# Kernel tuning notes

Measured on AMD Instinct MI355X. Metric: run time of the kernel, lower is better.

The kernel has to match this reference:

```python
import jax, jax.numpy as jnp
import numpy as np

N_NODES = 21
LN_EPS = 1e-5


def setup_inputs() -> dict:
    key = jax.random.key(0)
    ks = jax.random.split(key, 10)
    B, d, gh, E = 8192, 256, 512, 40
    h = jax.random.normal(ks[0], (B, N_NODES, d), dtype=jnp.float32)
    src_index = jax.random.randint(ks[1], (E,), 0, N_NODES)
    dst_index = jax.random.randint(ks[2], (E,), 0, N_NODES)
    # LayerNorm params
    ln_w = jnp.ones((d,), jnp.float32)
    ln_b = jnp.zeros((d,), jnp.float32)
    # value_proj: Linear(d, d), stored as (in, out)
    Wv = jax.random.normal(ks[3], (d, d), dtype=jnp.float32) / np.sqrt(d)
    bv = jax.random.normal(ks[4], (d,), dtype=jnp.float32) * 0.01
    # gate_mlp: Linear(2d, gh) -> GELU -> Linear(gh, 1)
    W1 = jax.random.normal(ks[5], (2 * d, gh), dtype=jnp.float32) / np.sqrt(2 * d)
    b1 = jax.random.normal(ks[6], (gh,), dtype=jnp.float32) * 0.01
    W2 = jax.random.normal(ks[7], (gh, 1), dtype=jnp.float32) / np.sqrt(gh)
    b2 = jax.random.normal(ks[8], (1,), dtype=jnp.float32) * 0.01
    return {"h": h, "src_index": src_index, "dst_index": dst_index,
            "ln_w": ln_w, "ln_b": ln_b, "Wv": Wv, "bv": bv,
            "W1": W1, "b1": b1, "W2": W2, "b2": b2}


def _layernorm(x, w, b):
    mu = jnp.mean(x, axis=-1, keepdims=True)
    var = jnp.mean(jnp.square(x - mu), axis=-1, keepdims=True)
    return (x - mu) * jax.lax.rsqrt(var + LN_EPS) * w + b


def reference(h, src_index, dst_index, ln_w, ln_b, Wv, bv, W1, b1, W2, b2):
    residual = h
    x = _layernorm(h, ln_w, ln_b)                      # (B, 21, d)
    src_feat = x[:, src_index, :]                      # (B, E, d) gather
    dst_feat = x[:, dst_index, :]                      # (B, E, d) gather
    values = jnp.einsum('bed,df->bef', src_feat, Wv) + bv  # (B, E, d)
    g = jnp.concatenate([src_feat, dst_feat], axis=-1) # (B, E, 2d)
    g = jax.nn.gelu(jnp.einsum('bec,ch->beh', g, W1) + b1, approximate=False)
    gates = jax.nn.sigmoid(jnp.einsum('beh,ho->beo', g, W2) + b2)  # (B, E, 1)
    messages = gates * values                          # (B, E, d)
    aggregated = jnp.zeros_like(x).at[:, dst_index, :].add(messages)  # scatter-add over nodes
    return residual + aggregated
```

## Files before the change

### kernel.cpp

```cpp
#include <hip/hip_runtime.h>
#include <hip/hip_bf16.h>
#include <math.h>

typedef __attribute__((ext_vector_type(8))) short short8;
typedef __attribute__((ext_vector_type(4))) float f32x4;

#define NN    21
#define DD    256
#define GH    512
#define NE    40
#define BT    3
#define MROWS (BT * NN)
#define MPAD  64
#define NTHR  256
#define UVSTR 36

__device__ __forceinline__ f32x4 mfma16(short8 a, short8 b, f32x4 c) {
    return __builtin_amdgcn_mfma_f32_16x16x32_bf16(a, b, c, 0, 0, 0);
}

__global__ void prep_weights(const float* __restrict__ Wv, const float* __restrict__ W1,
                             __hip_bfloat16* __restrict__ WvT,
                             __hip_bfloat16* __restrict__ WtT,
                             __hip_bfloat16* __restrict__ WbT) {
    __shared__ float tile[64][65];
    int bi = blockIdx.x;
    const float* src;
    int ld, tc, th;
    bool isW1 = bi < 64;
    if (isW1) { src = W1; ld = 512; tc = (bi & 7) * 64; th = (bi >> 3) * 64; }
    else      { int b = bi - 64; src = Wv; ld = 256; tc = (b & 3) * 64; th = (b >> 2) * 64; }
    for (int i = 0; i < 16; ++i) {
        int e = threadIdx.x + 256 * i;
        int r = e >> 6, cc = e & 63;
        tile[r][cc] = src[(size_t)(tc + r) * ld + th + cc];
    }
    __syncthreads();
    for (int i = 0; i < 16; ++i) {
        int e  = threadIdx.x + 256 * i;
        int r2 = e >> 6, cc2 = e & 63;
        float v = tile[cc2][r2];
        int hh = th + r2, c = tc + cc2;
        if (isW1) {
            if (c < 256) WtT[hh * 256 + c]         = __float2bfloat16(v);
            else         WbT[hh * 256 + (c - 256)] = __float2bfloat16(v);
        } else {
            WvT[hh * 256 + c] = __float2bfloat16(v);
        }
    }
}

__launch_bounds__(NTHR, 3)
__global__ void fused_kernel(const float* __restrict__ hin,
                             const int* __restrict__ srci, const int* __restrict__ dsti,
                             const float* __restrict__ lnw, const float* __restrict__ lnb,
                             const float* __restrict__ bv,  const float* __restrict__ b1,
                             const float* __restrict__ W2,  const float* __restrict__ b2,
                             const __hip_bfloat16* __restrict__ WvT,
                             const __hip_bfloat16* __restrict__ WtT,
                             const __hip_bfloat16* __restrict__ WbT,
                             float* __restrict__ out, int Btotal) {
    __shared__ __align__(16) char smem[32768];
    __shared__ float b1s[GH], w2s[GH], bvs[DD];
    __shared__ float gates[BT * NE];
    __shared__ int   srcs[NE], dsts[NE];
    __shared__ int   csr_off[NN + 1], csr_cur[NN], csr_eid[NE];

    const int tid  = threadIdx.x;
    const int lane = tid & 63;
    const int w    = tid >> 6;
    const int b0   = blockIdx.x * BT;

    if (tid < NE) { srcs[tid] = srci[tid]; dsts[tid] = dsti[tid]; }
    b1s[tid] = b1[tid];  b1s[tid + 256] = b1[tid + 256];
    w2s[tid] = W2[tid];  w2s[tid + 256] = W2[tid + 256];
    bvs[tid] = bv[tid];
    if (tid <= NN) csr_off[tid] = 0;
    int myd = (tid < NE) ? dsti[tid] : 0;
    __syncthreads();
    if (tid < NE) atomicAdd(&csr_off[myd + 1], 1);

    {
        float4 wgt = ((const float4*)lnw)[lane];
        float4 bta = ((const float4*)lnb)[lane];
        for (int r = w; r < MPAD; r += 4) {
            int b_loc = r / NN;
            int node  = r - b_loc * NN;
            bool valid = (r < MROWS) && (b0 + b_loc < Btotal);
            float4 h4 = {0.f, 0.f, 0.f, 0.f};
            if (valid)
                h4 = *(const float4*)(hin + ((size_t)(b0 + b_loc) * NN + node) * DD + lane * 4);
            float s  = h4.x + h4.y + h4.z + h4.w;
            float ss = h4.x*h4.x + h4.y*h4.y + h4.z*h4.z + h4.w*h4.w;
            for (int off = 32; off; off >>= 1) {
                s  += __shfl_xor(s,  off);
                ss += __shfl_xor(ss, off);
            }
            float mu   = s * (1.0f / 256.0f);
            float rstd = rsqrtf(ss * (1.0f / 256.0f) - mu * mu + 1e-5f);
            __align__(8) __hip_bfloat16 t[4];
            if (valid) {
                t[0] = __float2bfloat16((h4.x - mu) * rstd * wgt.x + bta.x);
                t[1] = __float2bfloat16((h4.y - mu) * rstd * wgt.y + bta.y);
                t[2] = __float2bfloat16((h4.z - mu) * rstd * wgt.z + bta.z);
                t[3] = __float2bfloat16((h4.w - mu) * rstd * wgt.w + bta.w);
            } else {
                __hip_bfloat16 z = __float2bfloat16(0.0f);
                t[0] = z; t[1] = z; t[2] = z; t[3] = z;
            }
            char* dst = smem + r * 512 + ((((lane >> 1) ^ (r & 7)) << 4) | ((lane & 1) << 3));
            *(ushort4*)dst = *(ushort4*)&t[0];
        }
    }
    __syncthreads();

    if (tid == 0) {
        for (int n = 0; n < NN; ++n) csr_off[n + 1] += csr_off[n];
        for (int n = 0; n < NN; ++n) csr_cur[n] = csr_off[n];
        for (int e = 0; e < NE; ++e) { int d = dsts[e]; csr_eid[csr_cur[d]++] = e; }
    }

    const int mq   = w & 1;
    const int nsel = w >> 1;
    const int l15  = lane & 15;
    const int lq   = lane >> 4;
    short8 afr[2][8];
    #pragma unroll
    for (int mt = 0; mt < 2; ++mt) {
        int r = 32 * mq + 16 * mt + l15;
        const char* rowp = smem + r * 512;
        int swz = r & 7;
        #pragma unroll
        for (int ki = 0; ki < 8; ++ki)
            afr[mt][ki] = *(const short8*)(rowp + ((((ki << 2) + lq) ^ swz) << 4));
    }
    __syncthreads();

    float* uvp = (float*)(smem + 16384);

    const bool gactive = tid < 2 * BT * NE;
    int rs = 0, rd = 0;
    if (gactive) {
        int p  = tid >> 1;
        int pb = p / NE, pe = p - pb * NE;
        rs = pb * NN + srcs[pe];
        rd = pb * NN + dsts[pe];
    }
    const int jh = tid & 1;

    #pragma unroll
    for (int i = 0; i < 4; ++i) {
        int v = tid + NTHR * i;
        int row = v >> 5, pg = v & 31;
        int cg = pg ^ (row & 7);
        const __hip_bfloat16* sp = (row < 16)
            ? (WtT + (size_t)row * 256 + cg * 8)
            : (WbT + (size_t)(row - 16) * 256 + cg * 8);
        *(float4*)(smem + row * 512 + pg * 16) = *(const float4*)sp;
    }
    __syncthreads();

    float gacc = 0.0f;
    const int   brow_r = 16 * nsel + l15;
    const char* browp  = smem + brow_r * 512;
    const int   bswz   = l15 & 7;
    for (int c = 0; c < 32; ++c) {
        f32x4 acc0 = {0.f,0.f,0.f,0.f}, acc1 = {0.f,0.f,0.f,0.f};
        #pragma unroll
        for (int ki = 0; ki < 8; ++ki) {
            short8 bf = *(const short8*)(browp + ((((ki << 2) + lq) ^ bswz) << 4));
            acc0 = mfma16(afr[0][ki], bf, acc0);
            acc1 = mfma16(afr[1][ki], bf, acc1);
        }
        #pragma unroll
        for (int r = 0; r < 4; ++r) {
            int col = 16 * nsel + l15;
            uvp[(32 * mq +      4 * lq + r) * UVSTR + col] = acc0[r];
            uvp[(32 * mq + 16 + 4 * lq + r) * UVSTR + col] = acc1[r];
        }
        __syncthreads();
        if (gactive) {
            const float* up  = uvp + rs * UVSTR + jh * 8;
            const float* vp  = uvp + rd * UVSTR + 16 + jh * 8;
            const float* b1p = b1s + c * 16 + jh * 8;
            const float* w2p = w2s + c * 16 + jh * 8;
            #pragma unroll
            for (int jj = 0; jj < 8; ++jj) {
                float z = up[jj] + vp[jj] + b1p[jj];
                float y = 1.5957691216f * (z + 0.044715f * z * z * z);
                float s = 1.0f / (1.0f + __expf(-y));
                gacc += z * s * w2p[jj];
            }
        }
        if (c + 1 < 32) {
            int cb = c + 1;
            #pragma unroll
            for (int i = 0; i < 4; ++i) {
                int v = tid + NTHR * i;
                int row = v >> 5, pg = v & 31;
                int cg = pg ^ (row & 7);
                const __hip_bfloat16* sp = (row < 16)
                    ? (WtT + (size_t)(cb * 16 + row) * 256 + cg * 8)
                    : (WbT + (size_t)(cb * 16 + row - 16) * 256 + cg * 8);
                *(float4*)(smem + row * 512 + pg * 16) = *(const float4*)sp;
            }
        }
        __syncthreads();
    }

    if (gactive) {
        float other = __shfl_xor(gacc, 1);
        if (jh == 0) {
            float tot = gacc + other + b2[0];
            gates[tid >> 1] = 1.0f / (1.0f + __expf(-tot));
        }
    }
    #pragma unroll
    for (int i = 0; i < 4; ++i) {
        int v = tid + NTHR * i;
        int row = v >> 5, pg = v & 31;
        int cg = pg ^ (row & 7);
        *(float4*)(smem + row * 512 + pg * 16) =
            *(const float4*)(WvT + (size_t)row * 256 + cg * 8);
    }
    __syncthreads();

    for (int vc = 0; vc < 8; ++vc) {
        f32x4 acc0 = {0.f,0.f,0.f,0.f}, acc1 = {0.f,0.f,0.f,0.f};
        #pragma unroll
        for (int ki = 0; ki < 8; ++ki) {
            short8 bf = *(const short8*)(browp + ((((ki << 2) + lq) ^ bswz) << 4));
            acc0 = mfma16(afr[0][ki], bf, acc0);
            acc1 = mfma16(afr[1][ki], bf, acc1);
        }
        #pragma unroll
        for (int r = 0; r < 4; ++r) {
            int col = 16 * nsel + l15;
            float bvv = bvs[vc * 32 + col];
            uvp[(32 * mq +      4 * lq + r) * UVSTR + col] = acc0[r] + bvv;
            uvp[(32 * mq + 16 + 4 * lq + r) * UVSTR + col] = acc1[r] + bvv;
        }
        __syncthreads();
        for (int q = tid; q < MROWS * 8; q += NTHR) {
            int row = q >> 3, g = q & 7;
            int b_loc = row / NN;
            int node  = row - b_loc * NN;
            if (b0 + b_loc < Btotal) {
                size_t ga = ((size_t)(b0 + b_loc) * NN + node) * DD + vc * 32 + g * 4;
                float4 hv = *(const float4*)(hin + ga);
                float a0 = hv.x, a1 = hv.y, a2 = hv.z, a3 = hv.w;
                int e1 = csr_off[node + 1];
                for (int ii = csr_off[node]; ii < e1; ++ii) {
                    int e  = csr_eid[ii];
                    float gv = gates[b_loc * NE + e];
                    const float* vp = uvp + (b_loc * NN + srcs[e]) * UVSTR + g * 4;
                    a0 += gv * vp[0]; a1 += gv * vp[1];
                    a2 += gv * vp[2]; a3 += gv * vp[3];
                }
                float4 o = {a0, a1, a2, a3};
                *(float4*)(out + ga) = o;
            }
        }
        if (vc + 1 < 8) {
            int vb = vc + 1;
            #pragma unroll
            for (int i = 0; i < 4; ++i) {
                int v = tid + NTHR * i;
                int row = v >> 5, pg = v & 31;
                int cg = pg ^ (row & 7);
                *(float4*)(smem + row * 512 + pg * 16) =
                    *(const float4*)(WvT + (size_t)(vb * 32 + row) * 256 + cg * 8);
            }
        }
        __syncthreads();
    }
}

extern "C" void kernel_launch(void* const* d_in, const int* in_sizes, int n_in,
                              void* d_out, int out_size, void* d_ws, size_t ws_size,
                              hipStream_t stream) {
    const float* h   = (const float*)d_in[0];
    const int*  srci = (const int*)d_in[1];
    const int*  dsti = (const int*)d_in[2];
    const float* lnw = (const float*)d_in[3];
    const float* lnb = (const float*)d_in[4];
    const float* Wv  = (const float*)d_in[5];
    const float* bv  = (const float*)d_in[6];
    const float* W1  = (const float*)d_in[7];
    const float* b1  = (const float*)d_in[8];
    const float* W2  = (const float*)d_in[9];
    const float* b2  = (const float*)d_in[10];
    float* out = (float*)d_out;

    __hip_bfloat16* WvT = (__hip_bfloat16*)d_ws;
    __hip_bfloat16* WtT = WvT + 256 * 256;
    __hip_bfloat16* WbT = WtT + 512 * 256;

    int Btotal = in_sizes[0] / (NN * DD);
    prep_weights<<<80, 256, 0, stream>>>(Wv, W1, WvT, WtT, WbT);
    int grid = (Btotal + BT - 1) / BT;
    fused_kernel<<<grid, NTHR, 0, stream>>>(h, srci, dsti, lnw, lnb, bv, b1, W2, b2,
                                            WvT, WtT, WbT, out, Btotal);
}
```

Measured before the change: 598.7 us.

## Prefetch next weight chunk into registers before MFMA loop and raise occupancy

The next chunk of bf16 weights is now loaded from global memory into registers at the top of each chunk iteration, so the load latency overlaps with the MFMA work, and it is written to shared memory after the barrier. The gate computation reads u/v, b1 and W2 with float4 vector loads, and the weight-staging addresses are precomputed once. Launch bounds go from 3 to 4 blocks per CU. The extra staging registers, together with the tighter register budget from the higher occupancy target, could cause spills.

```diff
diff --git a/kernel.cpp b/kernel.cpp
--- a/kernel.cpp
+++ b/kernel.cpp
@@ -50,7 +50,13 @@
     }
 }
 
-__launch_bounds__(NTHR, 3)
+#define GELU_GATE(zu, zv, zb, zw)  do {                              \
+    float z_ = (zu) + (zv) + (zb);                                   \
+    float y_ = 1.5957691216f * (z_ + 0.044715f * z_ * z_ * z_);      \
+    float s_ = 1.0f / (1.0f + __expf(-y_));                          \
+    gacc += z_ * s_ * (zw); } while (0)
+
+__launch_bounds__(NTHR, 4)
 __global__ void fused_kernel(const float* __restrict__ hin,
                              const int* __restrict__ srci, const int* __restrict__ dsti,
                              const float* __restrict__ lnw, const float* __restrict__ lnb,
@@ -61,7 +67,7 @@
                              const __hip_bfloat16* __restrict__ WbT,
                              float* __restrict__ out, int Btotal) {
     __shared__ __align__(16) char smem[32768];
-    __shared__ float b1s[GH], w2s[GH], bvs[DD];
+    __shared__ __align__(16) float b1s[GH], w2s[GH], bvs[DD];
     __shared__ float gates[BT * NE];
     __shared__ int   srcs[NE], dsts[NE];
     __shared__ int   csr_off[NN + 1], csr_cur[NN], csr_eid[NE];
@@ -79,6 +85,14 @@
     int myd = (tid < NE) ? dsti[tid] : 0;
     __syncthreads();
     if (tid < NE) atomicAdd(&csr_off[myd + 1], 1);
+
+    const int s_row0 = tid >> 5;
+    const int s_pg   = tid & 31;
+    const int s_cg   = s_pg ^ (s_row0 & 7);
+    char* const s_dst = smem + s_row0 * 512 + s_pg * 16;
+    const __hip_bfloat16* const s_wt = WtT + (size_t)s_row0 * 256 + s_cg * 8;
+    const __hip_bfloat16* const s_wb = WbT + (size_t)s_row0 * 256 + s_cg * 8;
+    const __hip_bfloat16* const s_wv = WvT + (size_t)s_row0 * 256 + s_cg * 8;
 
     {
         float4 wgt = ((const float4*)lnw)[lane];
@@ -148,15 +162,11 @@
     }
     const int jh = tid & 1;
 
-    #pragma unroll
-    for (int i = 0; i < 4; ++i) {
-        int v = tid + NTHR * i;
-        int row = v >> 5, pg = v & 31;
-        int cg = pg ^ (row & 7);
-        const __hip_bfloat16* sp = (row < 16)
-            ? (WtT + (size_t)row * 256 + cg * 8)
-            : (WbT + (size_t)(row - 16) * 256 + cg * 8);
-        *(float4*)(smem + row * 512 + pg * 16) = *(const float4*)sp;
+    {
+        *(float4*)(s_dst         ) = *(const float4*)(s_wt       );
+        *(float4*)(s_dst +  4096 ) = *(const float4*)(s_wt + 2048);
+        *(float4*)(s_dst +  8192 ) = *(const float4*)(s_wb       );
+        *(float4*)(s_dst + 12288 ) = *(const float4*)(s_wb + 2048);
     }
     __syncthreads();
 
@@ -165,6 +175,15 @@
     const char* browp  = smem + brow_r * 512;
     const int   bswz   = l15 & 7;
     for (int c = 0; c < 32; ++c) {
+        float4 stg0, stg1, stg2, stg3;
+        if (c + 1 < 32) {
+            const __hip_bfloat16* pt = s_wt + (size_t)(c + 1) * 4096;
+            const __hip_bfloat16* pb = s_wb + (size_t)(c + 1) * 4096;
+            stg0 = *(const float4*)(pt       );
+            stg1 = *(const float4*)(pt + 2048);
+            stg2 = *(const float4*)(pb       );
+            stg3 = *(const float4*)(pb + 2048);
+        }
         f32x4 acc0 = {0.f,0.f,0.f,0.f}, acc1 = {0.f,0.f,0.f,0.f};
         #pragma unroll
         for (int ki = 0; ki < 8; ++ki) {
@@ -179,31 +198,29 @@
             uvp[(32 * mq + 16 + 4 * lq + r) * UVSTR + col] = acc1[r];
         }
         __syncthreads();
+        if (c + 1 < 32) {
+            *(float4*)(s_dst        ) = stg0;
+            *(float4*)(s_dst +  4096) = stg1;
+            *(float4*)(s_dst +  8192) = stg2;
+            *(float4*)(s_dst + 12288) = stg3;
+        }
         if (gactive) {
-            const float* up  = uvp + rs * UVSTR + jh * 8;
-            const float* vp  = uvp + rd * UVSTR + 16 + jh * 8;
-            const float* b1p = b1s + c * 16 + jh * 8;
-            const float* w2p = w2s + c * 16 + jh * 8;
-            #pragma unroll
-            for (int jj = 0; jj < 8; ++jj) {
-                float z = up[jj] + vp[jj] + b1p[jj];
-                float y = 1.5957691216f * (z + 0.044715f * z * z * z);
-                float s = 1.0f / (1.0f + __expf(-y));
-                gacc += z * s * w2p[jj];
-            }
-        }
-        if (c + 1 < 32) {
-            int cb = c + 1;
-            #pragma unroll
-            for (int i = 0; i < 4; ++i) {
-                int v = tid + NTHR * i;
-                int row = v >> 5, pg = v & 31;
-                int cg = pg ^ (row & 7);
-                const __hip_bfloat16* sp = (row < 16)
-                    ? (WtT + (size_t)(cb * 16 + row) * 256 + cg * 8)
-                    : (WbT + (size_t)(cb * 16 + row - 16) * 256 + cg * 8);
-                *(float4*)(smem + row * 512 + pg * 16) = *(const float4*)sp;
-            }
+            const float4* up4 = (const float4*)(uvp + rs * UVSTR + jh * 8);
+            const float4* vp4 = (const float4*)(uvp + rd * UVSTR + 16 + jh * 8);
+            const float4* b14 = (const float4*)(b1s + c * 16 + jh * 8);
+            const float4* w24 = (const float4*)(w2s + c * 16 + jh * 8);
+            float4 ua = up4[0], ub = up4[1];
+            float4 va = vp4[0], vb = vp4[1];
+            float4 ba = b14[0], bb = b14[1];
+            float4 wa = w24[0], wb = w24[1];
+            GELU_GATE(ua.x, va.x, ba.x, wa.x);
+            GELU_GATE(ua.y, va.y, ba.y, wa.y);
+            GELU_GATE(ua.z, va.z, ba.z, wa.z);
+            GELU_GATE(ua.w, va.w, ba.w, wa.w);
+            GELU_GATE(ub.x, vb.x, bb.x, wb.x);
+            GELU_GATE(ub.y, vb.y, bb.y, wb.y);
+            GELU_GATE(ub.z, vb.z, bb.z, wb.z);
+            GELU_GATE(ub.w, vb.w, bb.w, wb.w);
         }
         __syncthreads();
     }
@@ -215,17 +232,23 @@
             gates[tid >> 1] = 1.0f / (1.0f + __expf(-tot));
         }
     }
-    #pragma unroll
-    for (int i = 0; i < 4; ++i) {
-        int v = tid + NTHR * i;
-        int row = v >> 5, pg = v & 31;
-        int cg = pg ^ (row & 7);
-        *(float4*)(smem + row * 512 + pg * 16) =
-            *(const float4*)(WvT + (size_t)row * 256 + cg * 8);
+    {
+        *(float4*)(s_dst        ) = *(const float4*)(s_wv       );
+        *(float4*)(s_dst +  4096) = *(const float4*)(s_wv + 2048);
+        *(float4*)(s_dst +  8192) = *(const float4*)(s_wv + 4096);
+        *(float4*)(s_dst + 12288) = *(const float4*)(s_wv + 6144);
     }
     __syncthreads();
 
     for (int vc = 0; vc < 8; ++vc) {
+        float4 stg0, stg1, stg2, stg3;
+        if (vc + 1 < 8) {
+            const __hip_bfloat16* pv = s_wv + (size_t)(vc + 1) * 8192;
+            stg0 = *(const float4*)(pv       );
+            stg1 = *(const float4*)(pv + 2048);
+            stg2 = *(const float4*)(pv + 4096);
+            stg3 = *(const float4*)(pv + 6144);
+        }
         f32x4 acc0 = {0.f,0.f,0.f,0.f}, acc1 = {0.f,0.f,0.f,0.f};
         #pragma unroll
         for (int ki = 0; ki < 8; ++ki) {
@@ -241,6 +264,12 @@
             uvp[(32 * mq + 16 + 4 * lq + r) * UVSTR + col] = acc1[r] + bvv;
         }
         __syncthreads();
+        if (vc + 1 < 8) {
+            *(float4*)(s_dst        ) = stg0;
+            *(float4*)(s_dst +  4096) = stg1;
+            *(float4*)(s_dst +  8192) = stg2;
+            *(float4*)(s_dst + 12288) = stg3;
+        }
         for (int q = tid; q < MROWS * 8; q += NTHR) {
             int row = q >> 3, g = q & 7;
             int b_loc = row / NN;
@@ -261,17 +290,6 @@
                 *(float4*)(out + ga) = o;
             }
         }
-        if (vc + 1 < 8) {
-            int vb = vc + 1;
-            #pragma unroll
-            for (int i = 0; i < 4; ++i) {
-                int v = tid + NTHR * i;
-                int row = v >> 5, pg = v & 31;
-                int cg = pg ^ (row & 7);
-                *(float4*)(smem + row * 512 + pg * 16) =
-                    *(const float4*)(WvT + (size_t)(vb * 32 + row) * 256 + cg * 8);
-            }
-        }
         __syncthreads();
     }
 }
```

New measurement: 530.3 us. -11.4%, faster.

## Load GEMM B fragments from global into registers with double-buffered uv scratch

Applied to the files above, without the earlier changes.

Weight tiles for the gate and value GEMMs are now loaded from global memory straight into register fragments, and the next chunk is prefetched while the current one runs on MFMA. This removes the LDS staging of weights. The uv output scratch is ping-ponged between two LDS regions, so each chunk needs one barrier instead of two. The GELU epilogue reads its operands as float4. The cost is higher register pressure from two 8-fragment buffers, and uncoalesced per-lane global loads of the weights, which rely on L1/L2 hits.

```diff
diff --git a/kernel.cpp b/kernel.cpp
--- a/kernel.cpp
+++ b/kernel.cpp
@@ -50,6 +50,12 @@
     }
 }
 
+#define GELU_GATE(zu, zv, zb, zw)  do {                              \
+    float z_ = (zu) + (zv) + (zb);                                   \
+    float y_ = 1.5957691216f * (z_ + 0.044715f * z_ * z_ * z_);      \
+    float s_ = 1.0f / (1.0f + __expf(-y_));                          \
+    gacc += z_ * s_ * (zw); } while (0)
+
 __launch_bounds__(NTHR, 3)
 __global__ void fused_kernel(const float* __restrict__ hin,
                              const int* __restrict__ srci, const int* __restrict__ dsti,
@@ -61,7 +67,7 @@
                              const __hip_bfloat16* __restrict__ WbT,
                              float* __restrict__ out, int Btotal) {
     __shared__ __align__(16) char smem[32768];
-    __shared__ float b1s[GH], w2s[GH], bvs[DD];
+    __shared__ __align__(16) float b1s[GH], w2s[GH], bvs[DD];
     __shared__ float gates[BT * NE];
     __shared__ int   srcs[NE], dsts[NE];
     __shared__ int   csr_off[NN + 1], csr_cur[NN], csr_eid[NE];
@@ -136,7 +142,8 @@
     }
     __syncthreads();
 
-    float* uvp = (float*)(smem + 16384);
+    float* const uv0 = (float*)smem;
+    float* const uv1 = (float*)(smem + 9216);
 
     const bool gactive = tid < 2 * BT * NE;
     int rs = 0, rd = 0;
@@ -146,66 +153,64 @@
         rs = pb * NN + srcs[pe];
         rd = pb * NN + dsts[pe];
     }
-    const int jh = tid & 1;
+    const int jh  = tid & 1;
+    const int col = 16 * nsel + l15;
+
+    const char* const bbase = ((const char*)(nsel ? WbT : WtT)) + l15 * 512 + lq * 16;
+    const char* const vbase = ((const char*)WvT) + (16 * nsel + l15) * 512 + lq * 16;
+
+    short8 bufA[8], bufB[8];
+
+    float gacc = 0.0f;
+
+#define P2_BODY(CX, BUFX, UVX, PREF, BUFY, CY)                                   \
+    {                                                                            \
+        if (PREF) {                                                              \
+            _Pragma("unroll")                                                    \
+            for (int ki = 0; ki < 8; ++ki)                                       \
+                BUFY[ki] = *(const short8*)(bbase + (CY) * 8192 + ki * 64);      \
+        }                                                                        \
+        f32x4 acc0 = {0.f,0.f,0.f,0.f}, acc1 = {0.f,0.f,0.f,0.f};                \
+        _Pragma("unroll")                                                        \
+        for (int ki = 0; ki < 8; ++ki) {                                         \
+            acc0 = mfma16(afr[0][ki], BUFX[ki], acc0);                           \
+            acc1 = mfma16(afr[1][ki], BUFX[ki], acc1);                           \
+        }                                                                        \
+        _Pragma("unroll")                                                        \
+        for (int r = 0; r < 4; ++r) {                                            \
+            UVX[(32 * mq +      4 * lq + r) * UVSTR + col] = acc0[r];            \
+            UVX[(32 * mq + 16 + 4 * lq + r) * UVSTR + col] = acc1[r];            \
+        }                                                                        \
+        __syncthreads();                                                         \
+        if (gactive) {                                                           \
+            const float4* up4 = (const float4*)(UVX + rs * UVSTR + jh * 8);      \
+            const float4* vp4 = (const float4*)(UVX + rd * UVSTR + 16 + jh * 8); \
+            const float4* b14 = (const float4*)(b1s + (CX) * 16 + jh * 8);       \
+            const float4* w24 = (const float4*)(w2s + (CX) * 16 + jh * 8);       \
+            float4 ua = up4[0], ub = up4[1];                                     \
+            float4 va = vp4[0], vb = vp4[1];                                     \
+            float4 ba = b14[0], bb = b14[1];                                     \
+            float4 wa = w24[0], wb = w24[1];                                     \
+            GELU_GATE(ua.x, va.x, ba.x, wa.x);                                   \
+            GELU_GATE(ua.y, va.y, ba.y, wa.y);                                   \
+            GELU_GATE(ua.z, va.z, ba.z, wa.z);                                   \
+            GELU_GATE(ua.w, va.w, ba.w, wa.w);                                   \
+            GELU_GATE(ub.x, vb.x, bb.x, wb.x);                                   \
+            GELU_GATE(ub.y, vb.y, bb.y, wb.y);                                   \
+            GELU_GATE(ub.z, vb.z, bb.z, wb.z);                                   \
+            GELU_GATE(ub.w, vb.w, bb.w, wb.w);                                   \
+        }                                                                        \
+    }
 
     #pragma unroll
-    for (int i = 0; i < 4; ++i) {
-        int v = tid + NTHR * i;
-        int row = v >> 5, pg = v & 31;
-        int cg = pg ^ (row & 7);
-        const __hip_bfloat16* sp = (row < 16)
-            ? (WtT + (size_t)row * 256 + cg * 8)
-            : (WbT + (size_t)(row - 16) * 256 + cg * 8);
-        *(float4*)(smem + row * 512 + pg * 16) = *(const float4*)sp;
-    }
-    __syncthreads();
-
-    float gacc = 0.0f;
-    const int   brow_r = 16 * nsel + l15;
-    const char* browp  = smem + brow_r * 512;
-    const int   bswz   = l15 & 7;
-    for (int c = 0; c < 32; ++c) {
-        f32x4 acc0 = {0.f,0.f,0.f,0.f}, acc1 = {0.f,0.f,0.f,0.f};
-        #pragma unroll
-        for (int ki = 0; ki < 8; ++ki) {
-            short8 bf = *(const short8*)(browp + ((((ki << 2) + lq) ^ bswz) << 4));
-            acc0 = mfma16(afr[0][ki], bf, acc0);
-            acc1 = mfma16(afr[1][ki], bf, acc1);
-        }
-        #pragma unroll
-        for (int r = 0; r < 4; ++r) {
-            int col = 16 * nsel + l15;
-            uvp[(32 * mq +      4 * lq + r) * UVSTR + col] = acc0[r];
-            uvp[(32 * mq + 16 + 4 * lq + r) * UVSTR + col] = acc1[r];
-        }
-        __syncthreads();
-        if (gactive) {
-            const float* up  = uvp + rs * UVSTR + jh * 8;
-            const float* vp  = uvp + rd * UVSTR + 16 + jh * 8;
-            const float* b1p = b1s + c * 16 + jh * 8;
-            const float* w2p = w2s + c * 16 + jh * 8;
-            #pragma unroll
-            for (int jj = 0; jj < 8; ++jj) {
-                float z = up[jj] + vp[jj] + b1p[jj];
-                float y = 1.5957691216f * (z + 0.044715f * z * z * z);
-                float s = 1.0f / (1.0f + __expf(-y));
-                gacc += z * s * w2p[jj];
-            }
-        }
-        if (c + 1 < 32) {
-            int cb = c + 1;
-            #pragma unroll
-            for (int i = 0; i < 4; ++i) {
-                int v = tid + NTHR * i;
-                int row = v >> 5, pg = v & 31;
-                int cg = pg ^ (row & 7);
-                const __hip_bfloat16* sp = (row < 16)
-                    ? (WtT + (size_t)(cb * 16 + row) * 256 + cg * 8)
-                    : (WbT + (size_t)(cb * 16 + row - 16) * 256 + cg * 8);
-                *(float4*)(smem + row * 512 + pg * 16) = *(const float4*)sp;
-            }
-        }
-        __syncthreads();
+    for (int ki = 0; ki < 8; ++ki)
+        bufA[ki] = *(const short8*)(bbase + ki * 64);
+
+    #pragma unroll 1
+    for (int it = 0; it < 16; ++it) {
+        const int c0 = 2 * it, c1 = 2 * it + 1;
+        P2_BODY(c0, bufA, uv0, true,      bufB, c1);
+        P2_BODY(c1, bufB, uv1, (it < 15), bufA, c1 + 1);
     }
 
     if (gactive) {
@@ -216,63 +221,59 @@
         }
     }
     #pragma unroll
-    for (int i = 0; i < 4; ++i) {
-        int v = tid + NTHR * i;
-        int row = v >> 5, pg = v & 31;
-        int cg = pg ^ (row & 7);
-        *(float4*)(smem + row * 512 + pg * 16) =
-            *(const float4*)(WvT + (size_t)row * 256 + cg * 8);
-    }
-    __syncthreads();
-
-    for (int vc = 0; vc < 8; ++vc) {
-        f32x4 acc0 = {0.f,0.f,0.f,0.f}, acc1 = {0.f,0.f,0.f,0.f};
-        #pragma unroll
-        for (int ki = 0; ki < 8; ++ki) {
-            short8 bf = *(const short8*)(browp + ((((ki << 2) + lq) ^ bswz) << 4));
-            acc0 = mfma16(afr[0][ki], bf, acc0);
-            acc1 = mfma16(afr[1][ki], bf, acc1);
-        }
-        #pragma unroll
-        for (int r = 0; r < 4; ++r) {
-            int col = 16 * nsel + l15;
-            float bvv = bvs[vc * 32 + col];
-            uvp[(32 * mq +      4 * lq + r) * UVSTR + col] = acc0[r] + bvv;
-            uvp[(32 * mq + 16 + 4 * lq + r) * UVSTR + col] = acc1[r] + bvv;
-        }
-        __syncthreads();
-        for (int q = tid; q < MROWS * 8; q += NTHR) {
-            int row = q >> 3, g = q & 7;
-            int b_loc = row / NN;
-            int node  = row - b_loc * NN;
-            if (b0 + b_loc < Btotal) {
-                size_t ga = ((size_t)(b0 + b_loc) * NN + node) * DD + vc * 32 + g * 4;
-                float4 hv = *(const float4*)(hin + ga);
-                float a0 = hv.x, a1 = hv.y, a2 = hv.z, a3 = hv.w;
-                int e1 = csr_off[node + 1];
-                for (int ii = csr_off[node]; ii < e1; ++ii) {
-                    int e  = csr_eid[ii];
-                    float gv = gates[b_loc * NE + e];
-                    const float* vp = uvp + (b_loc * NN + srcs[e]) * UVSTR + g * 4;
-                    a0 += gv * vp[0]; a1 += gv * vp[1];
-                    a2 += gv * vp[2]; a3 += gv * vp[3];
-                }
-                float4 o = {a0, a1, a2, a3};
-                *(float4*)(out + ga) = o;
-            }
-        }
-        if (vc + 1 < 8) {
-            int vb = vc + 1;
-            #pragma unroll
-            for (int i = 0; i < 4; ++i) {
-                int v = tid + NTHR * i;
-                int row = v >> 5, pg = v & 31;
-                int cg = pg ^ (row & 7);
-                *(float4*)(smem + row * 512 + pg * 16) =
-                    *(const float4*)(WvT + (size_t)(vb * 32 + row) * 256 + cg * 8);
-            }
-        }
-        __syncthreads();
+    for (int ki = 0; ki < 8; ++ki)
+        bufA[ki] = *(const short8*)(vbase + ki * 64);
+
+#define P4_BODY(VC, BUFX, UVX, PREF, BUFY, VY)                                   \
+    {                                                                            \
+        if (PREF) {                                                              \
+            _Pragma("unroll")                                                    \
+            for (int ki = 0; ki < 8; ++ki)                                       \
+                BUFY[ki] = *(const short8*)(vbase + (VY) * 16384 + ki * 64);     \
+        }                                                                        \
+        f32x4 acc0 = {0.f,0.f,0.f,0.f}, acc1 = {0.f,0.f,0.f,0.f};                \
+        _Pragma("unroll")                                                        \
+        for (int ki = 0; ki < 8; ++ki) {                                         \
+            acc0 = mfma16(afr[0][ki], BUFX[ki], acc0);                           \
+            acc1 = mfma16(afr[1][ki], BUFX[ki], acc1);                           \
+        }                                                                        \
+        {                                                                        \
+            float bvv = bvs[(VC) * 32 + col];                                    \
+            _Pragma("unroll")                                                    \
+            for (int r = 0; r < 4; ++r) {                                        \
+                UVX[(32 * mq +      4 * lq + r) * UVSTR + col] = acc0[r] + bvv;  \
+                UVX[(32 * mq + 16 + 4 * lq + r) * UVSTR + col] = acc1[r] + bvv;  \
+            }                                                                    \
+        }                                                                        \
+        __syncthreads();                                                         \
+        for (int q = tid; q < MROWS * 8; q += NTHR) {                            \
+            int row = q >> 3, g = q & 7;                                         \
+            int b_loc = row / NN;                                                \
+            int node  = row - b_loc * NN;                                        \
+            if (b0 + b_loc < Btotal) {                                           \
+                size_t ga = ((size_t)(b0 + b_loc) * NN + node) * DD              \
+                            + (VC) * 32 + g * 4;                                 \
+                float4 hv = *(const float4*)(hin + ga);                          \
+                float a0 = hv.x, a1 = hv.y, a2 = hv.z, a3 = hv.w;                \
+                int e1 = csr_off[node + 1];                                      \
+                for (int ii = csr_off[node]; ii < e1; ++ii) {                    \
+                    int e  = csr_eid[ii];                                        \
+                    float gv = gates[b_loc * NE + e];                            \
+                    const float* vp = UVX + (b_loc * NN + srcs[e]) * UVSTR + g * 4; \
+                    a0 += gv * vp[0]; a1 += gv * vp[1];                          \
+                    a2 += gv * vp[2]; a3 += gv * vp[3];                          \
+                }                                                                \
+                float4 o = {a0, a1, a2, a3};                                     \
+                *(float4*)(out + ga) = o;                                        \
+            }                                                                    \
+        }                                                                        \
+    }
+
+    #pragma unroll 1
+    for (int i2 = 0; i2 < 4; ++i2) {
+        const int v0 = 2 * i2, v1 = 2 * i2 + 1;
+        P4_BODY(v0, bufA, uv0, true,     bufB, v1);
+        P4_BODY(v1, bufB, uv1, (i2 < 3), bufA, v1 + 1);
     }
 }
 
```

Result: slower. 732.3 us (+22.3%).
